# Performance work log

Hardware: AMD Instinct MI355X
Metric: run time of the kernel (lower is better)

Reference implementation:

```python
import jax, jax.numpy as jnp
import numpy as np

T, C, NH, NL, NP = 5, 192, 4, 5, 4
DH = C // NH

def leaky(x):
    return jnp.where(x >= 0, x, 0.1 * x)

def conv2d(x, w, b, padding=1, dilation=1):
    out = jax.lax.conv_general_dilated(
        x, w, window_strides=(1, 1),
        padding=[(padding, padding), (padding, padding)],
        rhs_dilation=(dilation, dilation),
        dimension_numbers=('NCHW', 'OIHW', 'NCHW'))
    return out + b[None, :, None, None]

def grid_sample_border(img, gx, gy):
    # align_corners=True, padding_mode='border'; gx/gy normalized [-1,1], shape (B,H,W)
    B, Cc, H, W = img.shape
    x = jnp.clip((gx + 1.0) * 0.5 * (W - 1), 0.0, W - 1)
    y = jnp.clip((gy + 1.0) * 0.5 * (H - 1), 0.0, H - 1)
    x0 = jnp.floor(x); y0 = jnp.floor(y)
    wx = (x - x0).reshape(B, 1, -1); wy = (y - y0).reshape(B, 1, -1)
    flat = img.reshape(B, Cc, H * W)
    def g(yi, xi):
        xi = jnp.clip(xi, 0, W - 1).astype(jnp.int32)
        yi = jnp.clip(yi, 0, H - 1).astype(jnp.int32)
        return jnp.take_along_axis(flat, (yi * W + xi).reshape(B, 1, -1), axis=2)
    out = (g(y0, x0) * (1 - wx) * (1 - wy) + g(y0, x0 + 1) * wx * (1 - wy)
         + g(y0 + 1, x0) * (1 - wx) * wy + g(y0 + 1, x0 + 1) * wx * wy)
    return out.reshape(B, Cc, H, W)

def warp(x, flo):
    B, _, H, W = x.shape
    xx = jnp.arange(W, dtype=jnp.float32)[None, :] * jnp.ones((H, 1), jnp.float32)
    yy = jnp.arange(H, dtype=jnp.float32)[:, None] * jnp.ones((1, W), jnp.float32)
    gx = 2.0 * (xx[None] + flo[:, 0]) / max(W - 1, 1) - 1.0
    gy = 2.0 * (yy[None] + flo[:, 1]) / max(H - 1, 1) - 1.0
    return grid_sample_border(x, gx, gy)

def deform_sample(v_img, loc):
    # v_img (N,D,H,W); loc (N,Q,P,2) in [0,1]; bilinear, zeros padding, align_corners=False
    N, D, H, W = v_img.shape
    Q, P = loc.shape[1], loc.shape[2]
    x = loc[..., 0] * W - 0.5
    y = loc[..., 1] * H - 0.5
    x0 = jnp.floor(x); y0 = jnp.floor(y)
    wx = (x - x0).reshape(N, 1, -1); wy = (y - y0).reshape(N, 1, -1)
    flat = v_img.reshape(N, D, H * W)
    def g(yi, xi):
        valid = ((xi >= 0) & (xi <= W - 1) & (yi >= 0) & (yi <= H - 1)).astype(v_img.dtype)
        xi_c = jnp.clip(xi, 0, W - 1).astype(jnp.int32)
        yi_c = jnp.clip(yi, 0, H - 1).astype(jnp.int32)
        return jnp.take_along_axis(flat, (yi_c * W + xi_c).reshape(N, 1, -1), axis=2) * valid.reshape(N, 1, -1)
    out = (g(y0, x0) * (1 - wx) * (1 - wy) + g(y0, x0 + 1) * wx * (1 - wy)
         + g(y0 + 1, x0) * (1 - wx) * wy + g(y0 + 1, x0 + 1) * wx * wy)
    return out.reshape(N, D, Q, P)

def _forward(frame, srcframe, flow_forward, flow_backward,
             w_qk, b_qk, w_v, b_v, w_vproj, b_vproj, w_off, b_off,
             w_attn, b_attn, w_out, b_out, w_ff, b_ff,
             w_ffn1, b_ffn1, w_ffn2, b_ffn2):
    b, t, c, h, w = frame.shape
    ff01, ff12 = flow_forward[:, 0], flow_forward[:, 1]
    fb32, fb43 = flow_backward[:, 2], flow_backward[:, 3]
    ff02 = ff01 + warp(ff12, ff01)
    fb42 = fb43 + warp(fb32, fb43)
    warp02 = warp(frame[:, 0], ff02)
    warp12 = warp(frame[:, 1], ff12)
    warp32 = warp(frame[:, 3], fb32)
    warp42 = warp(frame[:, 4], fb42)
    qk_in = jnp.concatenate([warp02, warp12, frame[:, 2], warp32, warp42,
                             flow_forward.reshape(b, -1, h, w),
                             flow_backward.reshape(b, -1, h, w)], axis=1)
    queries = leaky(conv2d(qk_in, w_qk, b_qk)).reshape(b, t, c, h, w)
    value = leaky(conv2d(frame.reshape(b, t * c, h, w), w_v, b_v)).reshape(b, t, c, h, w)

    Lq = t * h * w
    q_tok = queries.transpose(0, 1, 3, 4, 2).reshape(b, Lq, c)
    v_tok = value.transpose(0, 1, 3, 4, 2).reshape(b, Lq, c)
    v_proj = (v_tok @ w_vproj.T + b_vproj).reshape(b, t, h * w, NH, DH)

    offs = (q_tok @ w_off.T + b_off).reshape(b, Lq, NH, NL, NP, 2)
    aw = (q_tok @ w_attn.T + b_attn).reshape(b, Lq, NH, NL * NP)
    aw = jax.nn.softmax(aw, axis=-1).reshape(b, Lq, NH, NL, NP)

    # reference points (all valid ratios are ones): ((x+0.5)/W, (y+0.5)/H)
    rx = (jnp.arange(w, dtype=frame.dtype) + 0.5) / w
    ry = (jnp.arange(h, dtype=frame.dtype) + 0.5) / h
    ref = jnp.stack(jnp.meshgrid(rx, ry, indexing='xy'), axis=-1).reshape(h * w, 2)
    ref = jnp.tile(ref, (t, 1))  # (Lq, 2)

    norm = jnp.array([w, h], dtype=frame.dtype)
    # flow-guided per-level displacement toward the center frame (level 2)
    zero = jnp.zeros_like(ff12)
    flows = jnp.stack([ff02, ff12, zero, fb32, fb42], axis=1)  # (b,NL,2,h,w)
    flow_norm = (flows / norm[None, None, :, None, None]).transpose(0, 1, 3, 4, 2).reshape(b, NL, h * w, 2)
    flow_norm = jnp.tile(flow_norm.transpose(0, 2, 1, 3), (1, t, 1, 1))  # (b,Lq,NL,2)

    loc = (ref[None, :, None, None, None, :]
           + offs / norm[None, None, None, None, None, :]
           + flow_norm[:, :, None, :, None, :])  # (b,Lq,NH,NL,NP,2)

    acc = jnp.zeros((b * NH, DH, Lq), dtype=frame.dtype)
    for l in range(NL):
        v_l = v_proj[:, l].transpose(0, 2, 3, 1).reshape(b * NH, DH, h, w)
        loc_l = loc[:, :, :, l].transpose(0, 2, 1, 3, 4).reshape(b * NH, Lq, NP, 2)
        samp = deform_sample(v_l, loc_l)  # (b*NH, DH, Lq, NP)
        w_l = aw[:, :, :, l].transpose(0, 2, 1, 3).reshape(b * NH, 1, Lq, NP)
        acc = acc + (samp * w_l).sum(-1)
    attn = acc.reshape(b, NH, DH, Lq).transpose(0, 3, 1, 2).reshape(b, Lq, c)
    attn = attn @ w_out.T + b_out

    out = attn.reshape(b, t, h, w, c).transpose(0, 1, 4, 2, 3).reshape(b * t, c, h, w)
    out = conv2d(out, w_ff, b_ff)
    out = out.reshape(b, t, c, h, w) + frame
    seq_in = jnp.concatenate([out.reshape(b * t, c, h, w), srcframe.reshape(b * t, c, h, w)], axis=1)
    ffn = conv2d(seq_in, w_ffn1, b_ffn1, padding=2, dilation=2)
    ffn = conv2d(leaky(ffn), w_ffn2, b_ffn2)
    out = out.reshape(b * t, c, h, w) + ffn
    return out.reshape(b, t, c, h, w)

def setup_inputs():
    key = jax.random.key(0)
    ks = jax.random.split(key, 16)
    B, H, W = 2, 64, 64
    s = 0.02
    d = {}
    d['frame'] = jax.random.normal(ks[0], (B, T, C, H, W), jnp.float32)
    d['srcframe'] = jax.random.normal(ks[1], (B, T, C, H, W), jnp.float32)
    d['flow_forward'] = jax.random.normal(ks[2], (B, 4, 2, H, W), jnp.float32)
    d['flow_backward'] = jax.random.normal(ks[3], (B, 4, 2, H, W), jnp.float32)
    cin_qk = T * C + 4 * (T - 1)
    d['w_qk'] = jax.random.normal(ks[4], (T * C, cin_qk, 3, 3), jnp.float32) * s
    d['b_qk'] = jnp.zeros((T * C,), jnp.float32)
    d['w_v'] = jax.random.normal(ks[5], (T * C, T * C, 3, 3), jnp.float32) * s
    d['b_v'] = jnp.zeros((T * C,), jnp.float32)
    d['w_vproj'] = jax.random.normal(ks[6], (C, C), jnp.float32) * s
    d['b_vproj'] = jnp.zeros((C,), jnp.float32)
    d['w_off'] = jax.random.normal(ks[7], (NH * NL * NP * 2, C), jnp.float32) * s
    d['b_off'] = jax.random.normal(ks[8], (NH * NL * NP * 2,), jnp.float32)
    d['w_attn'] = jax.random.normal(ks[9], (NH * NL * NP, C), jnp.float32) * s
    d['b_attn'] = jnp.zeros((NH * NL * NP,), jnp.float32)
    d['w_out'] = jax.random.normal(ks[10], (C, C), jnp.float32) * s
    d['b_out'] = jnp.zeros((C,), jnp.float32)
    d['w_ff'] = jax.random.normal(ks[11], (C, C, 3, 3), jnp.float32) * s
    d['b_ff'] = jnp.zeros((C,), jnp.float32)
    d['w_ffn1'] = jax.random.normal(ks[12], (C, 2 * C, 3, 3), jnp.float32) * s
    d['b_ffn1'] = jnp.zeros((C,), jnp.float32)
    d['w_ffn2'] = jax.random.normal(ks[13], (C, C, 3, 3), jnp.float32) * s
    d['b_ffn2'] = jnp.zeros((C,), jnp.float32)
    return d

def reference(frame, srcframe, flow_forward, flow_backward, w_qk, b_qk, w_v, b_v, w_vproj, b_vproj, w_off, b_off, w_attn, b_attn, w_out, b_out, w_ff, b_ff, w_ffn1, b_ffn1, w_ffn2, b_ffn2):
    out = _forward(frame, srcframe, flow_forward, flow_backward, w_qk, b_qk, w_v, b_v, w_vproj, b_vproj, w_off, b_off, w_attn, b_attn, w_out, b_out, w_ff, b_ff, w_ffn1, b_ffn1, w_ffn2, b_ffn2)
    return (out, srcframe)
```

## Files before the change

### kernel.cpp

```cpp
#include <hip/hip_runtime.h>


#define HWPX 4096
#define PPXN 4624
#define LQ   20480

typedef __attribute__((ext_vector_type(8))) short  short8;
typedef __attribute__((ext_vector_type(4))) short  short4v;
typedef __attribute__((ext_vector_type(4))) float  f32x4;
typedef __attribute__((ext_vector_type(4))) float  float4v;

__device__ __forceinline__ unsigned short f2bf(float f) {
    unsigned u = __float_as_uint(f);
    unsigned r = (u + 0x7FFF + ((u >> 16) & 1)) >> 16;
    return (unsigned short)r;
}
__device__ __forceinline__ float bf2f(unsigned short s) {
    return __uint_as_float(((unsigned)s) << 16);
}

__device__ __forceinline__ void gl_lds16(const unsigned short* g, unsigned short* l) {
    __builtin_amdgcn_global_load_lds(
        (const __attribute__((address_space(1))) unsigned int*)g,
        (__attribute__((address_space(3))) unsigned int*)l, 16, 0, 0);
}

__device__ __forceinline__ float bsample(const float* __restrict__ p, float sx, float sy) {
    sx = fminf(fmaxf(sx, 0.f), 63.f);
    sy = fminf(fmaxf(sy, 0.f), 63.f);
    float x0 = floorf(sx), y0 = floorf(sy);
    int ix0 = (int)x0, iy0 = (int)y0;
    int ix1 = ix0 < 63 ? ix0 + 1 : 63;
    int iy1 = iy0 < 63 ? iy0 + 1 : 63;
    float wx = sx - x0, wy = sy - y0;
    float v00 = p[iy0*64+ix0], v01 = p[iy0*64+ix1];
    float v10 = p[iy1*64+ix0], v11 = p[iy1*64+ix1];
    return (v00*(1.f-wx) + v01*wx)*(1.f-wy) + (v10*(1.f-wx) + v11*wx)*wy;
}

__device__ void dev_flow(int i, const float* __restrict__ ff,
                         const float* __restrict__ fb, float* __restrict__ flows) {
    int b = i >> 12, pix = i & 4095;
    int x = pix & 63, y = pix >> 6;
    const float* ff01 = ff + (size_t)(b*4+0)*2*HWPX;
    const float* ff12 = ff + (size_t)(b*4+1)*2*HWPX;
    const float* fb32 = fb + (size_t)(b*4+2)*2*HWPX;
    const float* fb43 = fb + (size_t)(b*4+3)*2*HWPX;
    float* F = flows + (size_t)b*5*2*HWPX;
    float ax = ff01[pix], ay = ff01[HWPX+pix];
    float sx = bsample(ff12,      (float)x+ax, (float)y+ay);
    float sy = bsample(ff12+HWPX, (float)x+ax, (float)y+ay);
    F[0*2*HWPX + pix]        = ax + sx;
    F[0*2*HWPX + HWPX + pix] = ay + sy;
    F[1*2*HWPX + pix]        = ff12[pix];
    F[1*2*HWPX + HWPX + pix] = ff12[HWPX+pix];
    F[2*2*HWPX + pix]        = 0.f;
    F[2*2*HWPX + HWPX + pix] = 0.f;
    F[3*2*HWPX + pix]        = fb32[pix];
    F[3*2*HWPX + HWPX + pix] = fb32[HWPX+pix];
    float bx = fb43[pix], by = fb43[HWPX+pix];
    float tx = bsample(fb32,      (float)x+bx, (float)y+by);
    float ty = bsample(fb32+HWPX, (float)x+bx, (float)y+by);
    F[4*2*HWPX + pix]        = bx + tx;
    F[4*2*HWPX + HWPX + pix] = by + ty;
}

__device__ void dev_wT(const float* __restrict__ w, unsigned short* __restrict__ wT,
                       int CI, int NKB, int cotile, int kblk, int tid) {
    unsigned short* dst = wT + ((size_t)(cotile*NKB + kblk))*18432;
    #pragma unroll
    for (int it = 0; it < 9; ++it) {
        int idx = it*256 + tid;
        int tap = idx >> 8, sub = idx & 255;
        int cg = sub >> 6, co = sub & 63;
        int cog = cotile*64 + co;
        int ci0 = kblk*32 + cg*8;
        short8 v;
        #pragma unroll
        for (int j = 0; j < 8; ++j) {
            int ci = ci0 + j;
            v[j] = (ci < CI) ? (short)f2bf(w[((size_t)cog*CI + ci)*9 + tap]) : (short)0;
        }
        *(short8*)(dst + (size_t)idx*8) = v;
    }
}

__device__ void dev_wg(const float* __restrict__ w1, const float* __restrict__ w2,
                       unsigned short* __restrict__ wg, int co_split, int CO,
                       int cotile, int tid) {
    unsigned short* dst = wg + (size_t)cotile*12288;
    #pragma unroll
    for (int it = 0; it < 6; ++it) {
        int idx = it*256 + tid;
        int kblk = idx >> 8, sub = idx & 255;
        int cg = sub >> 6, co = sub & 63;
        int cog = cotile*64 + co;
        int ci0 = kblk*32 + cg*8;
        short8 v = {};
        if (cog < CO) {
            const float* row = (cog < co_split) ? w1 + (size_t)cog*192
                                                : w2 + (size_t)(cog - co_split)*192;
            #pragma unroll
            for (int j = 0; j < 8; ++j) v[j] = (short)f2bf(row[ci0 + j]);
        }
        *(short8*)(dst + (size_t)idx*8) = v;
    }
}

__device__ void dev_pad(const float* __restrict__ in, unsigned short* __restrict__ outb,
                        int CI, int PITCH, int COFF, int img, int ppx_t, int cq, int tid) {
    int ppx = ppx_t*64 + (tid & 63);
    if (ppx >= PPXN) return;
    int c8 = (cq*4 + (tid >> 6))*8;
    unsigned short* dst = outb + ((size_t)img*PPXN + ppx)*PITCH;
    int py = ppx/68, pxc = ppx - py*68;
    if (py < 2 || py >= 66 || pxc < 2 || pxc >= 66) {
        short8 z = {};
        *(short8*)(dst + c8) = z;
        if (COFF) *(short8*)(dst + COFF + c8) = z;
        return;
    }
    int pix = ((py-2)<<6) + (pxc-2);
    short8 o;
    #pragma unroll
    for (int j = 0; j < 8; ++j)
        o[j] = (short)f2bf(in[((size_t)img*CI + c8 + j)*HWPX + pix]);
    *(short8*)(dst + COFF + c8) = o;
}

__global__ __launch_bounds__(256) void k_wprep(
    const float* __restrict__ flow_f, const float* __restrict__ flow_b,
    float* __restrict__ flows,
    const float* __restrict__ w_qk, unsigned short* __restrict__ wT_qk,
    const float* __restrict__ w_v,  unsigned short* __restrict__ wT_v,
    const float* __restrict__ w_ff, unsigned short* __restrict__ wT_ff,
    const float* __restrict__ w_f1, unsigned short* __restrict__ wT_f1,
    const float* __restrict__ w_f2, unsigned short* __restrict__ wT_f2,
    const float* __restrict__ w_vp, const float* __restrict__ w_off,
    const float* __restrict__ w_at, const float* __restrict__ w_out,
    unsigned short* __restrict__ wg_vp, unsigned short* __restrict__ wg_oa,
    unsigned short* __restrict__ wg_out,
    const float* __restrict__ srcframe, float* __restrict__ out2)
{
    int bid = blockIdx.x, tid = threadIdx.x;
    if (bid < 32) {
        dev_flow(bid*256 + tid, flow_f, flow_b, flows);
    } else if (bid < 497) {
        int p = bid - 32;   dev_wT(w_qk, wT_qk, 976, 31, p/31, p%31, tid);
    } else if (bid < 947) {
        int p = bid - 497;  dev_wT(w_v,  wT_v,  960, 30, p/30, p%30, tid);
    } else if (bid < 965) {
        int p = bid - 947;  dev_wT(w_ff, wT_ff, 192, 6,  p/6,  p%6,  tid);
    } else if (bid < 1001) {
        int p = bid - 965;  dev_wT(w_f1, wT_f1, 384, 12, p/12, p%12, tid);
    } else if (bid < 1019) {
        int p = bid - 1001; dev_wT(w_f2, wT_f2, 192, 6,  p/6,  p%6,  tid);
    } else if (bid < 1029) {
        int g = bid - 1019;
        if (g < 3)      dev_wg(w_vp,  nullptr, wg_vp, 192, 192, g,   tid);
        else if (g < 7) dev_wg(w_off, w_at,    wg_oa, 160, 240, g-3, tid);
        else            dev_wg(w_out, nullptr, wg_out, 192, 192, g-7, tid);
    } else {
        int c = bid - 1029;
        const float4v* s4 = (const float4v*)srcframe;
        float4v* d4 = (float4v*)out2;
        #pragma unroll
        for (int it = 0; it < 8; ++it) {
            int idx = it*245760 + c*256 + tid;
            d4[idx] = s4[idx];
        }
    }
}

__global__ void k_qkin(const unsigned short* __restrict__ Pv,
                       const float* __restrict__ ff, const float* __restrict__ fb,
                       const float* __restrict__ flows,
                       unsigned short* __restrict__ Pqk)
{
    int ppx = blockIdx.x*64 + threadIdx.x;
    if (ppx >= PPXN) return;
    int b = blockIdx.z;
    int c8 = (blockIdx.y*4 + threadIdx.y)*8;
    unsigned short* dst = Pqk + ((size_t)b*PPXN + ppx)*992 + c8;
    int py = ppx/68, pxc = ppx - py*68;
    short8 o = {};
    if (py >= 2 && py < 66 && pxc >= 2 && pxc < 66 && c8 < 976) {
        int y = py-2, x = pxc-2, pix = (y<<6)+x;
        if (c8 >= 960) {
            #pragma unroll
            for (int j = 0; j < 8; ++j) {
                int k = c8 - 960 + j;
                float v = (k < 8) ? ff[((size_t)b*8 + k)*HWPX + pix]
                                  : fb[((size_t)b*8 + k - 8)*HWPX + pix];
                o[j] = (short)f2bf(v);
            }
        } else {
            const unsigned short* Pvb = Pv + (size_t)b*PPXN*960;
            int slot = c8/192;
            if (slot == 2) {
                o = *(const short8*)(Pvb + (size_t)ppx*960 + c8);
            } else {
                const float* F = flows + ((size_t)(b*5 + slot)*2)*HWPX;
                float sx = fminf(fmaxf((float)x + F[pix], 0.f), 63.f);
                float sy = fminf(fmaxf((float)y + F[HWPX + pix], 0.f), 63.f);
                float x0 = floorf(sx), y0 = floorf(sy);
                int ix0 = (int)x0, iy0 = (int)y0;
                int ix1 = ix0 < 63 ? ix0+1 : 63, iy1 = iy0 < 63 ? iy0+1 : 63;
                float wx = sx - x0, wy = sy - y0;
                float w00 = (1.f-wx)*(1.f-wy), w01 = wx*(1.f-wy);
                float w10 = (1.f-wx)*wy,       w11 = wx*wy;
                short8 v00 = *(const short8*)(Pvb + ((size_t)((iy0+2)*68 + ix0+2))*960 + c8);
                short8 v01 = *(const short8*)(Pvb + ((size_t)((iy0+2)*68 + ix1+2))*960 + c8);
                short8 v10 = *(const short8*)(Pvb + ((size_t)((iy1+2)*68 + ix0+2))*960 + c8);
                short8 v11 = *(const short8*)(Pvb + ((size_t)((iy1+2)*68 + ix1+2))*960 + c8);
                #pragma unroll
                for (int j = 0; j < 8; ++j) {
                    float v = bf2f((unsigned short)v00[j])*w00 + bf2f((unsigned short)v01[j])*w01
                            + bf2f((unsigned short)v10[j])*w10 + bf2f((unsigned short)v11[j])*w11;
                    o[j] = (short)f2bf(v);
                }
            }
        }
    }
    *(short8*)dst = o;
}

__global__ void t_pad(const float* __restrict__ in, unsigned short* __restrict__ outb,
                      int CI, int PITCH, int COFF)
{
    int ppx = blockIdx.x*64 + threadIdx.x;
    if (ppx >= PPXN) return;
    int img = blockIdx.z;
    int c8 = (blockIdx.y*4 + threadIdx.y)*8;
    unsigned short* dst = outb + ((size_t)img*PPXN + ppx)*PITCH;
    int py = ppx/68, pxc = ppx - py*68;
    if (py < 2 || py >= 66 || pxc < 2 || pxc >= 66) {
        short8 z = {};
        *(short8*)(dst + c8) = z;
        if (COFF) *(short8*)(dst + COFF + c8) = z;
        return;
    }
    int pix = ((py-2)<<6) + (pxc-2);
    short8 o;
    #pragma unroll
    for (int j = 0; j < 8; ++j)
        o[j] = (short)f2bf(in[((size_t)img*CI + c8 + j)*HWPX + pix]);
    *(short8*)(dst + COFF + c8) = o;
}

template<int ROWS, int DIL, int OUTK, bool LEAKY, int RESK>
__global__ __launch_bounds__(256, 2) void k_conv(
    const unsigned short* __restrict__ P0, const unsigned short* __restrict__ P1,
    int CIP0, int CIP1, int NKB0, int NKB1,
    const unsigned short* __restrict__ wT0, const unsigned short* __restrict__ wT1,
    const float* __restrict__ bias0, const float* __restrict__ bias1,
    const float* __restrict__ resF, const unsigned short* __restrict__ resB, int resPitch,
    float* __restrict__ outF,
    unsigned short* __restrict__ outB0, unsigned short* __restrict__ outB1,
    int outPitch, int outCoff, int njobs)
{
    constexpr int RR     = ROWS*4 + 2*DIL;
    constexpr int XP     = 64 + 2*DIL;
    constexpr int PLANE  = RR*XP*16;
    constexpr int NCH    = RR*XP*4;
    constexpr int NXS    = (NCH + 255)/256;
    constexpr int TILEPX = ROWS*4*64;
    constexpr int SMEM_K = 4*PLANE + 36864;
    constexpr int SMEM_E = (OUTK <= 1) ? TILEPX*72*2 : 0;
    constexpr int SMEMSZ = SMEM_K > SMEM_E ? SMEM_K : SMEM_E;
    __shared__ __align__(16) unsigned char smem[SMEMSZ];
    unsigned char*  s_x = smem;
    unsigned short* s_w = (unsigned short*)(smem + 4*PLANE);

    int tid = threadIdx.x & 255;
    int gx = gridDim.x, gy = gridDim.y, gz = gridDim.z;
    int lin = blockIdx.x + gx*(blockIdx.y + gy*blockIdx.z);
    int tot = gx*gy*gz;
    if ((tot & 7) == 0) { int q = tot >> 3; lin = (lin & 7)*q + (lin >> 3); }
    int cotile = lin % gx; int rem = lin / gx;
    int ytile = rem % gy;  int z = rem / gy;

    int sel = (njobs == 2) ? (z >> 1) : 0;
    int img = (njobs == 2) ? (z & 1)  : z;
    const unsigned short* P  = sel ? P1  : P0;
    const unsigned short* wT = sel ? wT1 : wT0;
    const float* bias        = sel ? bias1 : bias0;
    unsigned short* outB     = sel ? outB1 : outB0;
    int CIP = sel ? CIP1 : CIP0;
    int NKB = sel ? NKB1 : NKB0;

    int y0 = ytile * (ROWS*4);
    const unsigned short* Pi = P + (size_t)img*PPXN*CIP;
    int w = tid >> 6, lane = tid & 63, lm = lane & 15, cig = lane >> 4;

    auto stage_x = [&](int kb) {
        int k0 = kb*32;
        #pragma unroll
        for (int it = 0; it < NXS; ++it) {
            int li = it*256 + tid;
            if (li < NCH) {
                int p = li / (RR*XP), rm = li - p*(RR*XP);
                int r = rm / XP, c = rm - r*XP;
                gl_lds16(Pi + ((size_t)((y0 + 2 - DIL + r)*68 + c + 2 - DIL))*CIP + k0 + p*8,
                         (unsigned short*)(s_x + li*16));
            }
        }
    };
    auto stage_w = [&](int kb) {
        const unsigned short* ws = wT + ((size_t)(cotile*NKB + kb))*18432;
        #pragma unroll
        for (int it = 0; it < 9; ++it)
            gl_lds16(ws + (size_t)(it*256+tid)*8, &s_w[(it*256+tid)*8]);
    };

    stage_x(0); stage_w(0);
    __syncthreads();

    f32x4 acc[4][ROWS*4] = {};
    for (int kb = 0; kb < NKB; ++kb) {
        __builtin_amdgcn_s_setprio(1);
        #pragma unroll
        for (int t = 0; t < 9; ++t) {
            int ky = t/3, kx = t - ky*3;
            short8 A[4];
            #pragma unroll
            for (int mb = 0; mb < 4; ++mb)
                A[mb] = *(const short8*)&s_w[((t*4 + cig)*64 + mb*16 + lm)*8];
            #pragma unroll
            for (int s = 0; s < ROWS; ++s) {
                short8 Bf[4];
                #pragma unroll
                for (int nc = 0; nc < 4; ++nc)
                    Bf[nc] = *(const short8*)&s_x[cig*PLANE +
                               ((w*ROWS + s + ky*DIL)*XP + nc*16 + lm + kx*DIL)*16];
                #pragma unroll
                for (int mb = 0; mb < 4; ++mb)
                    #pragma unroll
                    for (int nc = 0; nc < 4; ++nc)
                        acc[mb][s*4+nc] = __builtin_amdgcn_mfma_f32_16x16x32_bf16(
                            A[mb], Bf[nc], acc[mb][s*4+nc], 0, 0, 0);
            }
        }
        __builtin_amdgcn_s_setprio(0);
        __syncthreads();
        if (kb + 1 < NKB) { stage_x(kb+1); stage_w(kb+1); }
        __syncthreads();
    }

    if (OUTK == 0 || OUTK == 1) {
        unsigned short* epi = (unsigned short*)smem;
        #pragma unroll
        for (int mb = 0; mb < 4; ++mb) {
            int cob = cotile*64 + mb*16 + cig*4;
            int col = mb*16 + cig*4;
            #pragma unroll
            for (int s = 0; s < ROWS; ++s) {
                int lr = w*ROWS + s;
                #pragma unroll
                for (int nc = 0; nc < 4; ++nc) {
                    int x = nc*16 + lm;
                    int px_l = lr*64 + x;
                    int gpx = y0*64 + px_l;
                    short4v sv;
                    #pragma unroll
                    for (int r = 0; r < 4; ++r) {
                        float v = acc[mb][s*4+nc][r] + bias[cob + r];
                        if (LEAKY) v = v >= 0.f ? v : 0.1f*v;
                        if (RESK == 1) v += resF[((size_t)img*192 + cob + r)*HWPX + gpx];
                        sv[r] = (short)f2bf(v);
                    }
                    *(short4v*)&epi[px_l*72 + col] = sv;
                }
            }
        }
        __syncthreads();
        constexpr int NCPY = TILEPX/32;
        int slot = (OUTK == 0) ? (cotile*64)/192 : 0;
        int ccb  = (OUTK == 0) ? (cotile*64)%192 : (cotile*64 + outCoff);
        #pragma unroll
        for (int it2 = 0; it2 < NCPY; ++it2) {
            int li = it2*256 + tid;
            int px_l = li >> 3, sub = li & 7;
            short8 v = *(const short8*)&epi[px_l*72 + sub*8];
            int gpx = y0*64 + px_l;
            if (OUTK == 0) {
                *(short8*)(outB + ((size_t)(img*5 + slot)*HWPX + gpx)*192 + ccb + sub*8) = v;
            } else {
                int ppx = ((gpx>>6)+2)*68 + (gpx&63) + 2;
                *(short8*)(outB0 + ((size_t)img*PPXN + ppx)*outPitch + ccb + sub*8) = v;
            }
        }
    } else {
        #pragma unroll
        for (int mb = 0; mb < 4; ++mb) {
            int cob = cotile*64 + mb*16 + cig*4;
            #pragma unroll
            for (int s = 0; s < ROWS; ++s) {
                int y = y0 + w*ROWS + s;
                #pragma unroll
                for (int nc = 0; nc < 4; ++nc) {
                    int x = nc*16 + lm;
                    int px = (y<<6) + x;
                    int ppx = (y+2)*68 + x + 2;
                    short4v rv;
                    if (RESK == 2)
                        rv = *(const short4v*)(resB + ((size_t)img*PPXN + ppx)*resPitch + cob);
                    #pragma unroll
                    for (int r = 0; r < 4; ++r) {
                        float v = acc[mb][s*4+nc][r] + bias[cob + r];
                        if (LEAKY) v = v >= 0.f ? v : 0.1f*v;
                        if (RESK == 1) v += resF[((size_t)img*192 + cob + r)*HWPX + px];
                        if (RESK == 2) v += bf2f((unsigned short)rv[r]);
                        outF[((size_t)img*192 + cob + r)*HWPX + px] = v;
                    }
                }
            }
        }
    }
}

#define GEMM_CORE(Xi, WG_, cotile_)                                              \
    _Pragma("unroll")                                                            \
    for (int it = 0; it < 6; ++it)                                               \
        gl_lds16(WG_ + (size_t)(cotile_)*12288 + (it*256+tid)*8,                 \
                 &s_w[(it*256+tid)*8]);                                          \
    short8 xr[4];                                                                \
    _Pragma("unroll")                                                            \
    for (int it = 0; it < 4; ++it)                                               \
        xr[it] = *(const short8*)(Xi + (size_t)(px0 + tid)*192 + it*8);          \
    _Pragma("unroll")                                                            \
    for (int it = 0; it < 4; ++it)                                               \
        *(short8*)&s_x[0][it*4096 + tid*16] = xr[it];                            \
    __syncthreads();                                                             \
    int w = tid >> 6, lane = tid & 63, lm = lane & 15, cig = lane >> 4;          \
    f32x4 acc[4][4] = {};                                                        \
    int xb = 0;                                                                  \
    for (int kb = 0; kb < 6; ++kb) {                                             \
        bool pf = (kb < 5);                                                      \
        if (pf) {                                                                \
            int k0 = (kb+1)*32;                                                  \
            _Pragma("unroll")                                                    \
            for (int it = 0; it < 4; ++it)                                       \
                xr[it] = *(const short8*)(Xi + (size_t)(px0 + tid)*192 + k0 + it*8); \
        }                                                                        \
        short8 A[4], Bf[4];                                                      \
        _Pragma("unroll")                                                        \
        for (int nb = 0; nb < 4; ++nb)                                           \
            Bf[nb] = *(const short8*)&s_x[xb][cig*4096 + (w*64 + nb*16 + lm)*16];\
        _Pragma("unroll")                                                        \
        for (int mb = 0; mb < 4; ++mb)                                           \
            A[mb] = *(const short8*)&s_w[((kb*4 + cig)*64 + mb*16 + lm)*8];      \
        _Pragma("unroll")                                                        \
        for (int mb = 0; mb < 4; ++mb)                                           \
            _Pragma("unroll")                                                    \
            for (int nb = 0; nb < 4; ++nb)                                       \
                acc[mb][nb] = __builtin_amdgcn_mfma_f32_16x16x32_bf16(           \
                    A[mb], Bf[nb], acc[mb][nb], 0, 0, 0);                        \
        if (pf) {                                                                \
            _Pragma("unroll")                                                    \
            for (int it = 0; it < 4; ++it)                                       \
                *(short8*)&s_x[xb^1][it*4096 + tid*16] = xr[it];                 \
        }                                                                        \
        __syncthreads();                                                         \
        xb ^= 1;                                                                 \
    }

__global__ __launch_bounds__(256) void k_gemmA(
    const unsigned short* __restrict__ Xv, const unsigned short* __restrict__ WGv,
    const float* __restrict__ bvp, unsigned short* __restrict__ vp,
    const unsigned short* __restrict__ Xq, const unsigned short* __restrict__ WGq,
    const float* __restrict__ boff, const float* __restrict__ batt,
    float* __restrict__ offs, float* __restrict__ aw,
    unsigned short* __restrict__ P_ff, unsigned short* __restrict__ P_mid)
{
    __shared__ unsigned char  s_x[2][4*4096];
    __shared__ unsigned short s_w[12288];
    int tid = threadIdx.x & 255;
    int id = blockIdx.x;
    if (id < 480) {
        int cotile = id % 3, pxt = (id/3) % 16, img = id/48;
        int px0 = pxt*256;
        const unsigned short* Xi = Xv + (size_t)img*HWPX*192;
        GEMM_CORE(Xi, WGv, cotile)
        #pragma unroll
        for (int mb = 0; mb < 4; ++mb) {
            int cob = cotile*64 + mb*16 + cig*4;
            #pragma unroll
            for (int nb = 0; nb < 4; ++nb) {
                int px = px0 + w*64 + nb*16 + lm;
                short4v s;
                #pragma unroll
                for (int r = 0; r < 4; ++r)
                    s[r] = (short)f2bf(acc[mb][nb][r] + bvp[cob + r]);
                *(short4v*)(vp + ((size_t)img*HWPX + px)*192 + cob) = s;
            }
        }
    } else if (id < 1120) {
        int i2 = id - 480;
        int cotile = i2 % 4, pxt = (i2/4) % 16, img = i2/64;
        int px0 = pxt*256;
        const unsigned short* Xi = Xq + (size_t)img*HWPX*192;
        GEMM_CORE(Xi, WGq, cotile)
        int b = img/5, t = img - b*5;
        #pragma unroll
        for (int mb = 0; mb < 4; ++mb) {
            int cob = cotile*64 + mb*16 + cig*4;
            if (cob >= 240) continue;
            #pragma unroll
            for (int nb = 0; nb < 4; ++nb) {
                int px = px0 + w*64 + nb*16 + lm;
                #pragma unroll
                for (int r = 0; r < 4; ++r) {
                    int co = cob + r;
                    float bv = (co < 160) ? boff[co] : batt[co-160];
                    float v = acc[mb][nb][r] + bv;
                    if (co < 160) offs[((size_t)b*160 + co)*LQ + t*HWPX + px] = v;
                    else          aw[((size_t)b*80 + co-160)*LQ + t*HWPX + px] = v;
                }
            }
        }
    } else {
        int u = (id - 1120)*256 + tid;
        int c8i = u % 24; int r1 = u / 24;
        int b = r1 % 528; int r2 = r1 / 528;
        int img = r2 % 10; int buf = r2 / 10;
        int ppx;
        if (b < 136) ppx = b;
        else if (b < 272) ppx = 4488 + (b - 136);
        else { int b2 = b - 272; int row = 2 + (b2 >> 2); int cs = b2 & 3;
               ppx = row*68 + ((cs < 2) ? cs : cs + 64); }
        unsigned short* bp2 = buf ? P_mid : P_ff;
        short8 z = {};
        *(short8*)(bp2 + ((size_t)img*PPXN + ppx)*192 + c8i*8) = z;
    }
}

__global__ __launch_bounds__(256) void k_tailB(
    const unsigned short* __restrict__ X, const unsigned short* __restrict__ WG,
    const float* __restrict__ b1, unsigned short* __restrict__ P_ff,
    const float* __restrict__ srcframe, unsigned short* __restrict__ P_ffn1)
{
    __shared__ unsigned char  s_x[2][4*4096];
    __shared__ unsigned short s_w[12288];
    int tid = threadIdx.x & 255;
    int id = blockIdx.x;
    if (id < 480) {
        int cotile = id % 3, pxt = (id/3) % 16, img = id/48;
        int px0 = pxt*256;
        const unsigned short* Xi = X + (size_t)img*HWPX*192;
        GEMM_CORE(Xi, WG, cotile)
        #pragma unroll
        for (int mb = 0; mb < 4; ++mb) {
            int cob = cotile*64 + mb*16 + cig*4;
            #pragma unroll
            for (int nb = 0; nb < 4; ++nb) {
                int px = px0 + w*64 + nb*16 + lm;
                int ppx = ((px>>6)+2)*68 + (px&63) + 2;
                short4v s;
                #pragma unroll
                for (int r = 0; r < 4; ++r)
                    s[r] = (short)f2bf(acc[mb][nb][r] + b1[cob + r]);
                *(short4v*)(P_ff + ((size_t)img*PPXN + ppx)*192 + cob) = s;
            }
        }
    } else {
        int p = id - 480;
        int img = p / 438, rem = p - img*438;
        int ppx_t = rem % 73, cq = rem / 73;
        dev_pad(srcframe, P_ffn1, 192, 384, 192, img, ppx_t, cq, tid);
    }
}

__device__ __forceinline__ void addtap(float* acc, const unsigned short* __restrict__ src, float w) {
    const short8* s8 = (const short8*)src;
    #pragma unroll
    for (int q = 0; q < 6; ++q) {
        short8 v = s8[q];
        #pragma unroll
        for (int j = 0; j < 8; ++j)
            acc[q*8+j] += w * bf2f((unsigned short)v[j]);
    }
}

__global__ __launch_bounds__(256) void k_sample(
    const unsigned short* __restrict__ vp, const float* __restrict__ offs,
    const float* __restrict__ aw, const float* __restrict__ flows,
    unsigned short* __restrict__ accout)
{
    int blk = blockIdx.x;
    int b = blk / 320, sub = blk - b*320;
    int h = threadIdx.x >> 6;
    int lq = sub*64 + (threadIdx.x & 63);
    int pix = lq & 4095;
    int x = pix & 63, y = pix >> 6;
    const float* offp = offs + ((size_t)b*160 + h*40)*LQ + lq;
    const float* awp  = aw   + ((size_t)b*80  + h*20)*LQ + lq;
    float e[20];
    float m = -1e30f;
    #pragma unroll
    for (int j = 0; j < 20; ++j) { e[j] = awp[(size_t)j*LQ]; m = fmaxf(m, e[j]); }
    float ssum = 0.f;
    #pragma unroll
    for (int j = 0; j < 20; ++j) { e[j] = __expf(e[j]-m); ssum += e[j]; }
    float inv = 1.f/ssum;

    float acc[48];
    #pragma unroll
    for (int d = 0; d < 48; ++d) acc[d] = 0.f;

    for (int l = 0; l < 5; ++l) {
        float fx = flows[((size_t)(b*5+l)*2+0)*HWPX + pix];
        float fy = flows[((size_t)(b*5+l)*2+1)*HWPX + pix];
        const unsigned short* vpl = vp + ((size_t)(b*5+l)*HWPX)*192 + h*48;
        #pragma unroll
        for (int p = 0; p < 4; ++p) {
            int o = l*4 + p;
            float ox = offp[(size_t)(2*o)*LQ];
            float oy = offp[(size_t)(2*o+1)*LQ];
            float wv = e[o]*inv;
            float sx = (float)x + ox + fx;
            float sy = (float)y + oy + fy;
            float x0f = floorf(sx), y0f = floorf(sy);
            float wx = sx - x0f, wy = sy - y0f;
            int ix0 = (int)x0f, iy0 = (int)y0f;
            float w00 = wv*(1.f-wx)*(1.f-wy), w01 = wv*wx*(1.f-wy);
            float w10 = wv*(1.f-wx)*wy,       w11 = wv*wx*wy;
            bool vx0 = (ix0 >= 0)  && (ix0 <= 63);
            bool vx1 = (ix0 >= -1) && (ix0 <= 62);
            bool vy0 = (iy0 >= 0)  && (iy0 <= 63);
            bool vy1 = (iy0 >= -1) && (iy0 <= 62);
            if (vy0 && vx0) addtap(acc, vpl + (size_t)(iy0*64 + ix0)*192,       w00);
            if (vy0 && vx1) addtap(acc, vpl + (size_t)(iy0*64 + ix0 + 1)*192,   w01);
            if (vy1 && vx0) addtap(acc, vpl + (size_t)((iy0+1)*64 + ix0)*192,   w10);
            if (vy1 && vx1) addtap(acc, vpl + (size_t)((iy0+1)*64 + ix0+1)*192, w11);
        }
    }
    unsigned short* dst = accout + ((size_t)b*LQ + lq)*192 + h*48;
    #pragma unroll
    for (int q = 0; q < 6; ++q) {
        short8 s;
        #pragma unroll
        for (int j = 0; j < 8; ++j) s[j] = (short)f2bf(acc[q*8+j]);
        *(short8*)(dst + q*8) = s;
    }
}


extern "C" void kernel_launch(void* const* d_in, const int* in_sizes, int n_in,
                              void* d_out, int out_size, void* d_ws, size_t ws_size,
                              hipStream_t stream) {
    (void)in_sizes; (void)n_in; (void)out_size; (void)ws_size;
    const float* frame    = (const float*)d_in[0];
    const float* srcframe = (const float*)d_in[1];
    const float* flow_f   = (const float*)d_in[2];
    const float* flow_b   = (const float*)d_in[3];
    const float* w_qk  = (const float*)d_in[4];  const float* b_qk  = (const float*)d_in[5];
    const float* w_v   = (const float*)d_in[6];  const float* b_v   = (const float*)d_in[7];
    const float* w_vp  = (const float*)d_in[8];  const float* b_vp  = (const float*)d_in[9];
    const float* w_off = (const float*)d_in[10]; const float* b_off = (const float*)d_in[11];
    const float* w_at  = (const float*)d_in[12]; const float* b_at  = (const float*)d_in[13];
    const float* w_out = (const float*)d_in[14]; const float* b_out = (const float*)d_in[15];
    const float* w_ff  = (const float*)d_in[16]; const float* b_ff  = (const float*)d_in[17];
    const float* w_f1  = (const float*)d_in[18]; const float* b_f1  = (const float*)d_in[19];
    const float* w_f2  = (const float*)d_in[20]; const float* b_f2  = (const float*)d_in[21];
    float* out = (float*)d_out;
    char* W = (char*)d_ws;

    float*          flows  = (float*)(W + 0);
    unsigned short* wT_qk  = (unsigned short*)(W + 327680);
    unsigned short* wT_v   = (unsigned short*)(W + 17469440);
    unsigned short* P_qk   = (unsigned short*)(W + 34058240);
    unsigned short* P_ff   = P_qk;
    unsigned short* P_v    = (unsigned short*)(W + 52406272);
    unsigned short* P_mid  = P_v;
    unsigned short* Q_tok  = (unsigned short*)(W + 70162432);
    unsigned short* acc_tok= Q_tok;
    unsigned short* V_tok  = (unsigned short*)(W + 85891072);
    unsigned short* P_ffn1 = V_tok;
    unsigned short* vp     = (unsigned short*)(W + 101619712);
    float*          offs   = (float*)(W + 121403392);
    float*          aw     = (float*)(W + 147617792);
    unsigned short* wT_ff  = (unsigned short*)(W + 160724992);
    unsigned short* wT_f1  = (unsigned short*)(W + 161388544);
    unsigned short* wT_f2  = (unsigned short*)(W + 162715648);
    unsigned short* wg_vp  = (unsigned short*)(W + 163379200);
    unsigned short* wg_oa  = (unsigned short*)(W + 163452928);
    unsigned short* wg_out = (unsigned short*)(W + 163551232);

    dim3 bp(64, 4);

    k_wprep<<<1989, 256, 0, stream>>>(
        flow_f, flow_b, flows,
        w_qk, wT_qk, w_v, wT_v, w_ff, wT_ff, w_f1, wT_f1, w_f2, wT_f2,
        w_vp, w_off, w_at, w_out, wg_vp, wg_oa, wg_out,
        srcframe, out + (size_t)2*5*192*HWPX);
    t_pad<<<dim3(73,30,2), bp, 0, stream>>>(frame, P_v, 960, 960, 0);
    k_qkin<<<dim3(73,31,2), bp, 0, stream>>>(P_v, flow_f, flow_b, flows, P_qk);
    k_conv<2,1,0,true,0><<<dim3(15,8,4), 256, 0, stream>>>(
        P_qk, P_v, 992, 960, 31, 30, wT_qk, wT_v, b_qk, b_v,
        nullptr, nullptr, 0, nullptr, Q_tok, V_tok, 0, 0, 2);
    k_gemmA<<<2110, 256, 0, stream>>>(
        V_tok, wg_vp, b_vp, vp, Q_tok, wg_oa, b_off, b_at, offs, aw, P_ff, P_mid);
    k_sample<<<640, 256, 0, stream>>>(vp, offs, aw, flows, acc_tok);
    k_tailB<<<4860, 256, 0, stream>>>(acc_tok, wg_out, b_out, P_ff,
                                      srcframe, P_ffn1);
    k_conv<1,1,1,false,1><<<dim3(3,16,10), 256, 0, stream>>>(
        P_ff, nullptr, 192, 0, 6, 0, wT_ff, nullptr, b_ff, nullptr,
        frame, nullptr, 0, nullptr, P_ffn1, nullptr, 384, 0, 1);
    k_conv<1,2,1,true,0><<<dim3(3,16,10), 256, 0, stream>>>(
        P_ffn1, nullptr, 384, 0, 12, 0, wT_f1, nullptr, b_f1, nullptr,
        nullptr, nullptr, 0, nullptr, P_mid, nullptr, 192, 0, 1);
    k_conv<1,1,2,false,2><<<dim3(3,16,10), 256, 0, stream>>>(
        P_mid, nullptr, 192, 0, 6, 0, wT_f2, nullptr, b_f2, nullptr,
        nullptr, P_ffn1, 384, out, nullptr, nullptr, 0, 0, 1);
}
```

Baseline: 966.7 us.

## Store value projection head-major and split sampling threads across head halves

The value projection output is now written in a per-head layout (image, head, pixel, 48 channels) instead of pixel-major with 192 channels. The deformable sampling kernel assigns 8 threads per query (4 heads x 2 halves of 24 channels), doubling the grid and halving per-thread accumulators. This is meant to cut register pressure, raise occupancy and make each head's gathers hit a compact contiguous region. In exchange, the softmax and offset loads are recomputed by two threads per head, and the warp lanes now span fewer queries.

```diff
diff --git a/kernel.cpp b/kernel.cpp
--- a/kernel.cpp
+++ b/kernel.cpp
@@ -485,6 +485,7 @@
         #pragma unroll
         for (int mb = 0; mb < 4; ++mb) {
             int cob = cotile*64 + mb*16 + cig*4;
+            int h = cob/48, d = cob - h*48;
             #pragma unroll
             for (int nb = 0; nb < 4; ++nb) {
                 int px = px0 + w*64 + nb*16 + lm;
@@ -492,7 +493,7 @@
                 #pragma unroll
                 for (int r = 0; r < 4; ++r)
                     s[r] = (short)f2bf(acc[mb][nb][r] + bvp[cob + r]);
-                *(short4v*)(vp + ((size_t)img*HWPX + px)*192 + cob) = s;
+                *(short4v*)(vp + (((size_t)img*4 + h)*HWPX + px)*48 + d) = s;
             }
         }
     } else if (id < 1120) {
@@ -571,14 +572,14 @@
     }
 }
 
-__device__ __forceinline__ void addtap(float* acc, const unsigned short* __restrict__ src, float w) {
+__device__ __forceinline__ void addtap24(float* acc, const unsigned short* __restrict__ src, float w) {
     const short8* s8 = (const short8*)src;
     #pragma unroll
-    for (int q = 0; q < 6; ++q) {
-        short8 v = s8[q];
+    for (int u = 0; u < 3; ++u) {
+        short8 v = s8[u];
         #pragma unroll
         for (int j = 0; j < 8; ++j)
-            acc[q*8+j] += w * bf2f((unsigned short)v[j]);
+            acc[u*8+j] += w * bf2f((unsigned short)v[j]);
     }
 }
 
@@ -588,9 +589,10 @@
     unsigned short* __restrict__ accout)
 {
     int blk = blockIdx.x;
-    int b = blk / 320, sub = blk - b*320;
-    int h = threadIdx.x >> 6;
-    int lq = sub*64 + (threadIdx.x & 63);
+    int b = blk / 640, sub = blk - b*640;
+    int tid = threadIdx.x;
+    int lq = sub*32 + (tid >> 3);
+    int h = (tid >> 1) & 3, q = tid & 1;
     int pix = lq & 4095;
     int x = pix & 63, y = pix >> 6;
     const float* offp = offs + ((size_t)b*160 + h*40)*LQ + lq;
@@ -604,14 +606,14 @@
     for (int j = 0; j < 20; ++j) { e[j] = __expf(e[j]-m); ssum += e[j]; }
     float inv = 1.f/ssum;
 
-    float acc[48];
-    #pragma unroll
-    for (int d = 0; d < 48; ++d) acc[d] = 0.f;
+    float acc[24];
+    #pragma unroll
+    for (int d = 0; d < 24; ++d) acc[d] = 0.f;
 
     for (int l = 0; l < 5; ++l) {
         float fx = flows[((size_t)(b*5+l)*2+0)*HWPX + pix];
         float fy = flows[((size_t)(b*5+l)*2+1)*HWPX + pix];
-        const unsigned short* vpl = vp + ((size_t)(b*5+l)*HWPX)*192 + h*48;
+        const unsigned short* vpl = vp + (((size_t)(b*5+l)*4 + h)*HWPX)*48 + q*24;
         #pragma unroll
         for (int p = 0; p < 4; ++p) {
             int o = l*4 + p;
@@ -629,19 +631,19 @@
             bool vx1 = (ix0 >= -1) && (ix0 <= 62);
             bool vy0 = (iy0 >= 0)  && (iy0 <= 63);
             bool vy1 = (iy0 >= -1) && (iy0 <= 62);
-            if (vy0 && vx0) addtap(acc, vpl + (size_t)(iy0*64 + ix0)*192,       w00);
-            if (vy0 && vx1) addtap(acc, vpl + (size_t)(iy0*64 + ix0 + 1)*192,   w01);
-            if (vy1 && vx0) addtap(acc, vpl + (size_t)((iy0+1)*64 + ix0)*192,   w10);
-            if (vy1 && vx1) addtap(acc, vpl + (size_t)((iy0+1)*64 + ix0+1)*192, w11);
-        }
-    }
-    unsigned short* dst = accout + ((size_t)b*LQ + lq)*192 + h*48;
-    #pragma unroll
-    for (int q = 0; q < 6; ++q) {
+            if (vy0 && vx0) addtap24(acc, vpl + (size_t)(iy0*64 + ix0)*48,       w00);
+            if (vy0 && vx1) addtap24(acc, vpl + (size_t)(iy0*64 + ix0 + 1)*48,   w01);
+            if (vy1 && vx0) addtap24(acc, vpl + (size_t)((iy0+1)*64 + ix0)*48,   w10);
+            if (vy1 && vx1) addtap24(acc, vpl + (size_t)((iy0+1)*64 + ix0+1)*48, w11);
+        }
+    }
+    unsigned short* dst = accout + ((size_t)b*LQ + lq)*192 + h*48 + q*24;
+    #pragma unroll
+    for (int u = 0; u < 3; ++u) {
         short8 s;
         #pragma unroll
-        for (int j = 0; j < 8; ++j) s[j] = (short)f2bf(acc[q*8+j]);
-        *(short8*)(dst + q*8) = s;
+        for (int j = 0; j < 8; ++j) s[j] = (short)f2bf(acc[u*8+j]);
+        *(short8*)(dst + u*8) = s;
     }
 }
 
@@ -701,7 +703,7 @@
         nullptr, nullptr, 0, nullptr, Q_tok, V_tok, 0, 0, 2);
     k_gemmA<<<2110, 256, 0, stream>>>(
         V_tok, wg_vp, b_vp, vp, Q_tok, wg_oa, b_off, b_at, offs, aw, P_ff, P_mid);
-    k_sample<<<640, 256, 0, stream>>>(vp, offs, aw, flows, acc_tok);
+    k_sample<<<1280, 256, 0, stream>>>(vp, offs, aw, flows, acc_tok);
     k_tailB<<<4860, 256, 0, stream>>>(acc_tok, wg_out, b_out, P_ff,
                                       srcframe, P_ffn1);
     k_conv<1,1,1,false,1><<<dim3(3,16,10), 256, 0, stream>>>(
```

New measurement: 807.8 us. 16.4% less time.
